# Kernel tuning notes

Hardware: AMD Instinct MI355X
Metric: run time of the kernel (lower is better)

## Reference

```python
import jax, jax.numpy as jnp
import numpy as np

N_NODES = 100000
N_EDGES = 20000  # hyperedges
NNZ = 800000
D = 128


def setup_inputs() -> dict:
    key = jax.random.key(0)
    ks = jax.random.split(key, 10)
    X = jax.random.normal(ks[0], (N_NODES, D), dtype=jnp.float32)
    X0 = jax.random.normal(ks[1], (N_NODES, D), dtype=jnp.float32)
    degE = jax.random.uniform(ks[2], (N_EDGES, 1), dtype=jnp.float32)
    degV = jax.random.uniform(ks[3], (N_NODES, 1), dtype=jnp.float32)
    alpha = jax.random.uniform(ks[4], (1,), dtype=jnp.float32)
    beta = jax.random.uniform(ks[5], (1,), dtype=jnp.float32)
    W_w = jax.random.normal(ks[6], (D, D), dtype=jnp.float32) / np.sqrt(D)
    g1_src = jax.random.randint(ks[7], (NNZ,), 0, N_NODES, dtype=jnp.int64 if jax.config.read('jax_enable_x64') else jnp.int32)
    g1_dst = jax.random.randint(ks[8], (NNZ,), 0, N_EDGES)
    g2_src = jax.random.randint(ks[9], (NNZ,), 0, N_EDGES)
    g2_dst = jax.random.randint(jax.random.fold_in(key, 99), (NNZ,), 0, N_NODES)
    return {"X": X, "X0": X0, "degE": degE, "degV": degV, "alpha": alpha,
            "beta": beta, "W_w": W_w, "g1_src": g1_src, "g1_dst": g1_dst,
            "g2_src": g2_src, "g2_dst": g2_dst}


def reference(X, X0, degE, degV, alpha, beta, W_w, g1_src, g1_dst, g2_src, g2_dst):
    n_edges = degE.shape[0]
    n_nodes = degV.shape[0]
    a = alpha[0]
    b = beta[0]
    # copy_u_sum(g1, X): gather node rows, scatter-sum into hyperedges
    Xe = jax.ops.segment_sum(X[g1_src], g1_dst, num_segments=n_edges)  # [E, D]
    Xe = Xe * degE
    # copy_u_sum(g2, Xe): gather hyperedge rows, scatter-sum into nodes
    Xv = jax.ops.segment_sum(Xe[g2_src], g2_dst, num_segments=n_nodes)  # [N, D]
    Xv = Xv * degV
    # GCNII-style initial residual + identity mapping
    Xi = (1.0 - a) * Xv + a * X0
    out = (1.0 - b) * Xi + b * (Xi @ W_w.T)  # Linear(bias=False)
    return out
```

## Files before the change

### kernel.cpp

```cpp
#include <hip/hip_runtime.h>

#define DD 128
#define SCAN_CHUNK 2048
#define PAD1 16
#define PAD2 8

typedef __attribute__((ext_vector_type(8))) _Float16 f16x8;
typedef __attribute__((ext_vector_type(4))) _Float16 f16x4;
typedef __attribute__((ext_vector_type(4))) float f32x4;

__global__ __launch_bounds__(256)
void k_hist1(const int* __restrict__ g1d, int* __restrict__ cnt1p,
             int* __restrict__ rank1, int nnz, int no, int hb,
             const float* __restrict__ W, const float* __restrict__ betaP,
             _Float16* __restrict__ Mh,
             const float* __restrict__ X, _Float16* __restrict__ Xh, int nx) {
    const int b = blockIdx.x;
    if (b < hb) {
        int q = b * 256 + threadIdx.x;
        if (q >= no) return;
        int i = q << 3;
        if (i + 8 <= nnz) {
            int4 d0 = *(const int4*)(g1d + i);
            int4 d1 = *(const int4*)(g1d + i + 4);
            int r0 = atomicAdd(&cnt1p[d0.x * PAD1], 1);
            int r1 = atomicAdd(&cnt1p[d0.y * PAD1], 1);
            int r2 = atomicAdd(&cnt1p[d0.z * PAD1], 1);
            int r3 = atomicAdd(&cnt1p[d0.w * PAD1], 1);
            int r4 = atomicAdd(&cnt1p[d1.x * PAD1], 1);
            int r5 = atomicAdd(&cnt1p[d1.y * PAD1], 1);
            int r6 = atomicAdd(&cnt1p[d1.z * PAD1], 1);
            int r7 = atomicAdd(&cnt1p[d1.w * PAD1], 1);
            *(int4*)(rank1 + i)     = make_int4(r0, r1, r2, r3);
            *(int4*)(rank1 + i + 4) = make_int4(r4, r5, r6, r7);
        } else {
            for (; i < nnz; ++i) rank1[i] = atomicAdd(&cnt1p[g1d[i] * PAD1], 1);
        }
        return;
    }
    if (b < hb + 8) {
        int gid = (b - hb) * 256 + threadIdx.x;
        if (gid >= DD * DD / 8) return;
        int c  = gid >> 4;
        int k0 = (gid & 15) << 3;
        float bb = betaP[0], ib = 1.0f - bb;
        const float* p = W + c * DD + k0;
        float4 lo = *(const float4*)p, hi = *(const float4*)(p + 4);
        float v[8] = {lo.x, lo.y, lo.z, lo.w, hi.x, hi.y, hi.z, hi.w};
        f16x8 t;
        #pragma unroll
        for (int j = 0; j < 8; ++j) {
            float m = bb * v[j] + ((k0 + j) == c ? ib : 0.0f);
            t[j] = (_Float16)m;
        }
        *(f16x8*)(Mh + (size_t)c * DD + k0) = t;
        return;
    }
    int gid = (b - hb - 8) * 256 + threadIdx.x;
    int i = gid << 3;
    if (i + 8 <= nx) {
        float4 lo = *(const float4*)(X + i);
        float4 hi = *(const float4*)(X + i + 4);
        f16x8 t;
        t[0] = (_Float16)lo.x; t[1] = (_Float16)lo.y;
        t[2] = (_Float16)lo.z; t[3] = (_Float16)lo.w;
        t[4] = (_Float16)hi.x; t[5] = (_Float16)hi.y;
        t[6] = (_Float16)hi.z; t[7] = (_Float16)hi.w;
        *(f16x8*)(Xh + i) = t;
    } else {
        for (; i < nx; ++i) Xh[i] = (_Float16)X[i];
    }
}

__global__ __launch_bounds__(256)
void k_scan_blocks(const int* __restrict__ cnt, int* __restrict__ off,
                   int* __restrict__ bsum, int n, int str) {
    __shared__ int sh[256];
    const int tid = threadIdx.x;
    const int base = blockIdx.x * SCAN_CHUNK + tid * 8;
    int v[8];
    int s = 0;
    #pragma unroll
    for (int j = 0; j < 8; ++j) {
        int idx = base + j;
        v[j] = (idx < n) ? cnt[(size_t)idx * str] : 0;
        s += v[j];
    }
    sh[tid] = s;
    __syncthreads();
    for (int d = 1; d < 256; d <<= 1) {
        int y = (tid >= d) ? sh[tid - d] : 0;
        __syncthreads();
        sh[tid] += y;
        __syncthreads();
    }
    int incl = sh[tid];
    int run = incl - s;
    #pragma unroll
    for (int j = 0; j < 8; ++j) {
        int idx = base + j;
        if (idx < n) off[idx] = run;
        run += v[j];
    }
    if (tid == 255) bsum[blockIdx.x] = incl;
}

__global__ __launch_bounds__(256)
void k_scan_add(int* __restrict__ off, const int* __restrict__ bsum,
                int n, int nnz) {
    int gid = blockIdx.x * 256 + threadIdx.x;
    if (gid == 0) off[n] = nnz;
    if (gid >= n) return;
    int chunk = gid >> 11;
    int p = 0;
    for (int i = 0; i < chunk; ++i) p += bsum[i];
    off[gid] += p;
}

__global__ __launch_bounds__(256)
void k_fill(const int* __restrict__ dst, const int* __restrict__ src,
            const int* __restrict__ off, const int* __restrict__ rank,
            int* __restrict__ out, int nnz) {
    int q = blockIdx.x * 256 + threadIdx.x;
    int i = q << 2;
    if (i + 4 <= nnz) {
        int4 d = *(const int4*)(dst + i);
        int4 s = *(const int4*)(src + i);
        int4 r = *(const int4*)(rank + i);
        int o0 = off[d.x];
        int o1 = off[d.y];
        int o2 = off[d.z];
        int o3 = off[d.w];
        out[o0 + r.x] = s.x;
        out[o1 + r.y] = s.y;
        out[o2 + r.z] = s.z;
        out[o3 + r.w] = s.w;
    } else {
        for (; i < nnz; ++i) out[off[dst[i]] + rank[i]] = src[i];
    }
}

__global__ __launch_bounds__(256)
void k_h2_egather(const int* __restrict__ g2d, int* __restrict__ cnt2p,
                  int* __restrict__ rank2, int nnz, int no, int H,
                  const _Float16* __restrict__ Xh, const int* __restrict__ off1,
                  const int* __restrict__ srcs1, const float* __restrict__ degE,
                  _Float16* __restrict__ XeH, int n_edges) {
    if (blockIdx.x < H) {
        int q = blockIdx.x * 256 + threadIdx.x;
        if (q >= no) return;
        int i = q << 3;
        if (i + 8 <= nnz) {
            int4 d0 = *(const int4*)(g2d + i);
            int4 d1 = *(const int4*)(g2d + i + 4);
            int r0 = atomicAdd(&cnt2p[d0.x * PAD2], 1);
            int r1 = atomicAdd(&cnt2p[d0.y * PAD2], 1);
            int r2 = atomicAdd(&cnt2p[d0.z * PAD2], 1);
            int r3 = atomicAdd(&cnt2p[d0.w * PAD2], 1);
            int r4 = atomicAdd(&cnt2p[d1.x * PAD2], 1);
            int r5 = atomicAdd(&cnt2p[d1.y * PAD2], 1);
            int r6 = atomicAdd(&cnt2p[d1.z * PAD2], 1);
            int r7 = atomicAdd(&cnt2p[d1.w * PAD2], 1);
            *(int4*)(rank2 + i)     = make_int4(r0, r1, r2, r3);
            *(int4*)(rank2 + i + 4) = make_int4(r4, r5, r6, r7);
        } else {
            for (; i < nnz; ++i) rank2[i] = atomicAdd(&cnt2p[g2d[i] * PAD2], 1);
        }
        return;
    }
    int gid = (blockIdx.x - H) * 256 + threadIdx.x;
    int e = gid >> 4;
    if (e >= n_edges) return;
    int k = (gid & 15) << 3;
    int beg = off1[e], end = off1[e + 1];
    float a0[8] = {0, 0, 0, 0, 0, 0, 0, 0};
    float a1[8] = {0, 0, 0, 0, 0, 0, 0, 0};
    int j = beg;
    for (; j + 8 <= end; j += 8) {
        int s0 = srcs1[j + 0];
        int s1 = srcs1[j + 1];
        int s2 = srcs1[j + 2];
        int s3 = srcs1[j + 3];
        int s4 = srcs1[j + 4];
        int s5 = srcs1[j + 5];
        int s6 = srcs1[j + 6];
        int s7 = srcs1[j + 7];
        f16x8 v0 = *(const f16x8*)(Xh + (size_t)s0 * DD + k);
        f16x8 v1 = *(const f16x8*)(Xh + (size_t)s1 * DD + k);
        f16x8 v2 = *(const f16x8*)(Xh + (size_t)s2 * DD + k);
        f16x8 v3 = *(const f16x8*)(Xh + (size_t)s3 * DD + k);
        f16x8 v4 = *(const f16x8*)(Xh + (size_t)s4 * DD + k);
        f16x8 v5 = *(const f16x8*)(Xh + (size_t)s5 * DD + k);
        f16x8 v6 = *(const f16x8*)(Xh + (size_t)s6 * DD + k);
        f16x8 v7 = *(const f16x8*)(Xh + (size_t)s7 * DD + k);
        #pragma unroll
        for (int t = 0; t < 8; ++t) {
            a0[t] += (float)v0[t] + (float)v2[t];
            a1[t] += (float)v1[t] + (float)v3[t];
        }
        #pragma unroll
        for (int t = 0; t < 8; ++t) {
            a0[t] += (float)v4[t] + (float)v6[t];
            a1[t] += (float)v5[t] + (float)v7[t];
        }
    }
    for (; j < end; ++j) {
        int s = srcs1[j];
        f16x8 v = *(const f16x8*)(Xh + (size_t)s * DD + k);
        #pragma unroll
        for (int t = 0; t < 8; ++t) a0[t] += (float)v[t];
    }
    float f = degE[e];
    f16x8 ob;
    #pragma unroll
    for (int t = 0; t < 8; ++t) ob[t] = (_Float16)(f * (a0[t] + a1[t]));
    *(f16x8*)(XeH + (size_t)e * DD + k) = ob;
}

__global__ __launch_bounds__(256)
void k_node_gather(const _Float16* __restrict__ XeH, const int* __restrict__ off,
                   const int* __restrict__ srcs, const float* __restrict__ degV,
                   const float* __restrict__ X0, const float* __restrict__ alphaP,
                   float* __restrict__ Xi, int n_nodes) {
    int gid = blockIdx.x * 256 + threadIdx.x;
    int v = gid >> 5;
    if (v >= n_nodes) return;
    int k = (gid & 31) << 2;
    int beg = off[v], end = off[v + 1];
    float4 acc0 = {0, 0, 0, 0}, acc1 = {0, 0, 0, 0};
    int j = beg;
    for (; j + 4 <= end; j += 4) {
        int s0 = srcs[j + 0];
        int s1 = srcs[j + 1];
        int s2 = srcs[j + 2];
        int s3 = srcs[j + 3];
        f16x4 h0 = *(const f16x4*)(XeH + (size_t)s0 * DD + k);
        f16x4 h1 = *(const f16x4*)(XeH + (size_t)s1 * DD + k);
        f16x4 h2 = *(const f16x4*)(XeH + (size_t)s2 * DD + k);
        f16x4 h3 = *(const f16x4*)(XeH + (size_t)s3 * DD + k);
        acc0.x += (float)h0[0]; acc0.y += (float)h0[1]; acc0.z += (float)h0[2]; acc0.w += (float)h0[3];
        acc1.x += (float)h1[0]; acc1.y += (float)h1[1]; acc1.z += (float)h1[2]; acc1.w += (float)h1[3];
        acc0.x += (float)h2[0]; acc0.y += (float)h2[1]; acc0.z += (float)h2[2]; acc0.w += (float)h2[3];
        acc1.x += (float)h3[0]; acc1.y += (float)h3[1]; acc1.z += (float)h3[2]; acc1.w += (float)h3[3];
    }
    for (; j < end; ++j) {
        int s = srcs[j];
        f16x4 h = *(const f16x4*)(XeH + (size_t)s * DD + k);
        acc0.x += (float)h[0]; acc0.y += (float)h[1]; acc0.z += (float)h[2]; acc0.w += (float)h[3];
    }
    float a = alphaP[0];
    float f = (1.0f - a) * degV[v];
    float4 x0 = *(const float4*)(X0 + (size_t)v * DD + k);
    float4 o;
    o.x = f * (acc0.x + acc1.x) + a * x0.x;
    o.y = f * (acc0.y + acc1.y) + a * x0.y;
    o.z = f * (acc0.z + acc1.z) + a * x0.z;
    o.w = f * (acc0.w + acc1.w) + a * x0.w;
    *(float4*)(Xi + (size_t)v * DD + k) = o;
}

__global__ __launch_bounds__(256)
void k_gemm_mfma(float* xio, const _Float16* __restrict__ Mh, int n_rows) {
    const int lane = threadIdx.x & 63;
    const int wid  = threadIdx.x >> 6;
    const int m16  = lane & 15;
    const int quad = lane >> 4;
    const int kq   = quad * 8;

    const int strip = blockIdx.x * 4 + wid;
    const int row0 = strip * 16;
    if (row0 >= n_rows) return;

    int arow = row0 + m16;
    if (arow >= n_rows) arow = n_rows - 1;
    const float* xr = xio + (size_t)arow * DD;

    f16x8 af[4];
    #pragma unroll
    for (int kf = 0; kf < 4; ++kf) {
        const float* p = xr + kf * 32 + kq;
        float4 lo = *(const float4*)p;
        float4 hi = *(const float4*)(p + 4);
        f16x8 t;
        t[0] = (_Float16)lo.x; t[1] = (_Float16)lo.y;
        t[2] = (_Float16)lo.z; t[3] = (_Float16)lo.w;
        t[4] = (_Float16)hi.x; t[5] = (_Float16)hi.y;
        t[6] = (_Float16)hi.z; t[7] = (_Float16)hi.w;
        af[kf] = t;
    }

    #pragma unroll
    for (int nt = 0; nt < 8; ++nt) {
        const _Float16* mr = Mh + (size_t)(nt * 16 + m16) * DD + kq;
        f32x4 acc = {0.f, 0.f, 0.f, 0.f};
        #pragma unroll
        for (int kf = 0; kf < 4; ++kf) {
            f16x8 bfrag = *(const f16x8*)(mr + kf * 32);
            acc = __builtin_amdgcn_mfma_f32_16x16x32_f16(af[kf], bfrag, acc, 0, 0, 0);
        }
        const int col = nt * 16 + m16;
        #pragma unroll
        for (int r = 0; r < 4; ++r) {
            int row = row0 + quad * 4 + r;
            if (row < n_rows)
                xio[(size_t)row * DD + col] = acc[r];
        }
    }
}

extern "C" void kernel_launch(void* const* d_in, const int* in_sizes, int n_in,
                              void* d_out, int out_size, void* d_ws, size_t ws_size,
                              hipStream_t stream) {
    const float* X     = (const float*)d_in[0];
    const float* X0    = (const float*)d_in[1];
    const float* degE  = (const float*)d_in[2];
    const float* degV  = (const float*)d_in[3];
    const float* alpha = (const float*)d_in[4];
    const float* beta  = (const float*)d_in[5];
    const float* W     = (const float*)d_in[6];
    const int*   g1s   = (const int*)d_in[7];
    const int*   g1d   = (const int*)d_in[8];
    const int*   g2s   = (const int*)d_in[9];
    const int*   g2d   = (const int*)d_in[10];
    float* out = (float*)d_out;

    const int n_nodes = in_sizes[3];
    const int n_edges = in_sizes[2];
    const int nnz     = in_sizes[7];
    const int nx      = n_nodes * DD;

    int*   wsi   = (int*)d_ws;
    _Float16* XeH = (_Float16*)d_ws;
    size_t o     = (size_t)n_edges * DD / 2;
    int*   rank1 = wsi + o;
    int*   rank2 = rank1;
    o += nnz;
    int*   off1  = wsi + o;          o += n_edges + 1;
    int*   off2  = wsi + o;          o += n_nodes + 1;
    size_t srcs_base = o;
    int*   srcs1 = wsi + o;          o += nnz;
    int*   srcs2 = wsi + o;          o += nnz;
    int*   bsum  = wsi + o;          o += 64;
    _Float16* Mh = (_Float16*)(wsi + o); o += DD * DD / 2;
    int*   cnt1p = wsi + srcs_base;
    int*   cnt2p = wsi + srcs_base + nnz;
    _Float16* Xh = (_Float16*)d_out;

    hipMemsetAsync(cnt1p, 0, 2 * (size_t)nnz * sizeof(int), stream);

    const int nb1 = (n_edges + SCAN_CHUNK - 1) / SCAN_CHUNK;
    const int nb2 = (n_nodes + SCAN_CHUNK - 1) / SCAN_CHUNK;
    const int no  = (nnz + 7) / 8;
    const int hb  = (no + 255) / 256;
    const int cb  = (nx / 8 + 255) / 256;
    const int nq  = (nnz + 3) / 4;
    const int qb  = (nq + 255) / 256;

    k_hist1<<<hb + 8 + cb, 256, 0, stream>>>(g1d, cnt1p, rank1, nnz, no, hb,
                                             W, beta, Mh, X, Xh, nx);
    k_scan_blocks<<<nb1, 256, 0, stream>>>(cnt1p, off1, bsum, n_edges, PAD1);
    k_scan_add<<<(n_edges + 255) / 256, 256, 0, stream>>>(off1, bsum, n_edges, nnz);
    k_fill<<<qb, 256, 0, stream>>>(g1d, g1s, off1, rank1, srcs1, nnz);

    const int egb = (n_edges * 16 + 255) / 256;
    k_h2_egather<<<hb + egb, 256, 0, stream>>>(g2d, cnt2p, rank2, nnz, no, hb,
                                               Xh, off1, srcs1, degE, XeH, n_edges);

    k_scan_blocks<<<nb2, 256, 0, stream>>>(cnt2p, off2, bsum, n_nodes, PAD2);
    k_scan_add<<<(n_nodes + 255) / 256, 256, 0, stream>>>(off2, bsum, n_nodes, nnz);
    k_fill<<<qb, 256, 0, stream>>>(g2d, g2s, off2, rank2, srcs2, nnz);

    k_node_gather<<<(n_nodes * 32 + 255) / 256, 256, 0, stream>>>(
        XeH, off2, srcs2, degV, X0, alpha, out, n_nodes);

    const int nstrips = (n_nodes + 15) / 16;
    k_gemm_mfma<<<(nstrips + 3) / 4, 256, 0, stream>>>(out, Mh, n_nodes);
}
```

Before: 374.8 us.

## Fuse node gather into MFMA GEMM, drop scan-add passes, wave-per-edge gather

Removes both k_scan_add kernels: each consumer block now builds the block-prefix array from bsum in shared memory and adds it to the local scan offsets. The node gather is fused into the MFMA GEMM. Each wave accumulates a 16-row strip, writes Xi as fp16 into swizzled LDS and feeds the MFMA directly, so the fp32 Xi round trip through global memory goes away. The edge gather changes from 16 lanes per edge to a full wave per edge, with four sub-groups reduced by shuffles. Costs are a serial per-block prefix loop, less parallelism per node in the gather (4 lanes per row), and extra register pressure from 32 accumulators.

```diff
diff --git a/kernel.cpp b/kernel.cpp
--- a/kernel.cpp
+++ b/kernel.cpp
@@ -99,44 +99,41 @@
     #pragma unroll
     for (int j = 0; j < 8; ++j) {
         int idx = base + j;
-        if (idx < n) off[idx] = run;
+        if (idx <= n) off[idx] = run;
         run += v[j];
     }
     if (tid == 255) bsum[blockIdx.x] = incl;
-}
-
-__global__ __launch_bounds__(256)
-void k_scan_add(int* __restrict__ off, const int* __restrict__ bsum,
-                int n, int nnz) {
-    int gid = blockIdx.x * 256 + threadIdx.x;
-    if (gid == 0) off[n] = nnz;
-    if (gid >= n) return;
-    int chunk = gid >> 11;
-    int p = 0;
-    for (int i = 0; i < chunk; ++i) p += bsum[i];
-    off[gid] += p;
 }
 
 __global__ __launch_bounds__(256)
 void k_fill(const int* __restrict__ dst, const int* __restrict__ src,
             const int* __restrict__ off, const int* __restrict__ rank,
+            const int* __restrict__ bsum, int nb,
             int* __restrict__ out, int nnz) {
+    __shared__ int pref[64];
+    if (threadIdx.x == 0) {
+        int run = 0;
+        for (int i = 0; i < nb; ++i) { pref[i] = run; run += bsum[i]; }
+        pref[nb] = run;
+    }
+    __syncthreads();
     int q = blockIdx.x * 256 + threadIdx.x;
     int i = q << 2;
     if (i + 4 <= nnz) {
         int4 d = *(const int4*)(dst + i);
         int4 s = *(const int4*)(src + i);
         int4 r = *(const int4*)(rank + i);
-        int o0 = off[d.x];
-        int o1 = off[d.y];
-        int o2 = off[d.z];
-        int o3 = off[d.w];
+        int o0 = off[d.x] + pref[d.x >> 11];
+        int o1 = off[d.y] + pref[d.y >> 11];
+        int o2 = off[d.z] + pref[d.z >> 11];
+        int o3 = off[d.w] + pref[d.w >> 11];
         out[o0 + r.x] = s.x;
         out[o1 + r.y] = s.y;
         out[o2 + r.z] = s.z;
         out[o3 + r.w] = s.w;
     } else {
-        for (; i < nnz; ++i) out[off[dst[i]] + rank[i]] = src[i];
+        for (; i < nnz; ++i)
+            out[off[dst[i]] + pref[dst[i] >> 11] + rank[i]] = src[i];
     }
 }
 
@@ -144,6 +141,7 @@
 void k_h2_egather(const int* __restrict__ g2d, int* __restrict__ cnt2p,
                   int* __restrict__ rank2, int nnz, int no, int H,
                   const _Float16* __restrict__ Xh, const int* __restrict__ off1,
+                  const int* __restrict__ bsum1, int nb1,
                   const int* __restrict__ srcs1, const float* __restrict__ degE,
                   _Float16* __restrict__ XeH, int n_edges) {
     if (blockIdx.x < H) {
@@ -168,127 +166,167 @@
         }
         return;
     }
-    int gid = (blockIdx.x - H) * 256 + threadIdx.x;
-    int e = gid >> 4;
+    __shared__ int pref[16];
+    if (threadIdx.x == 0) {
+        int run = 0;
+        for (int i = 0; i < nb1; ++i) { pref[i] = run; run += bsum1[i]; }
+        pref[nb1] = run;
+    }
+    __syncthreads();
+    const int wid  = threadIdx.x >> 6;
+    const int lane = threadIdx.x & 63;
+    int e = (blockIdx.x - H) * 4 + wid;
     if (e >= n_edges) return;
-    int k = (gid & 15) << 3;
-    int beg = off1[e], end = off1[e + 1];
+    const int g = lane >> 4;
+    const int c = lane & 15;
+    int beg = off1[e] + pref[e >> 11];
+    int end = off1[e + 1] + pref[(e + 1) >> 11];
     float a0[8] = {0, 0, 0, 0, 0, 0, 0, 0};
     float a1[8] = {0, 0, 0, 0, 0, 0, 0, 0};
-    int j = beg;
-    for (; j + 8 <= end; j += 8) {
-        int s0 = srcs1[j + 0];
-        int s1 = srcs1[j + 1];
-        int s2 = srcs1[j + 2];
-        int s3 = srcs1[j + 3];
-        int s4 = srcs1[j + 4];
-        int s5 = srcs1[j + 5];
-        int s6 = srcs1[j + 6];
-        int s7 = srcs1[j + 7];
-        f16x8 v0 = *(const f16x8*)(Xh + (size_t)s0 * DD + k);
-        f16x8 v1 = *(const f16x8*)(Xh + (size_t)s1 * DD + k);
-        f16x8 v2 = *(const f16x8*)(Xh + (size_t)s2 * DD + k);
-        f16x8 v3 = *(const f16x8*)(Xh + (size_t)s3 * DD + k);
-        f16x8 v4 = *(const f16x8*)(Xh + (size_t)s4 * DD + k);
-        f16x8 v5 = *(const f16x8*)(Xh + (size_t)s5 * DD + k);
-        f16x8 v6 = *(const f16x8*)(Xh + (size_t)s6 * DD + k);
-        f16x8 v7 = *(const f16x8*)(Xh + (size_t)s7 * DD + k);
-        #pragma unroll
-        for (int t = 0; t < 8; ++t) {
-            a0[t] += (float)v0[t] + (float)v2[t];
-            a1[t] += (float)v1[t] + (float)v3[t];
-        }
-        #pragma unroll
-        for (int t = 0; t < 8; ++t) {
-            a0[t] += (float)v4[t] + (float)v6[t];
-            a1[t] += (float)v5[t] + (float)v7[t];
-        }
-    }
-    for (; j < end; ++j) {
+    int j = beg + g;
+    for (; j + 4 < end; j += 8) {
+        int s0 = srcs1[j];
+        int s1 = srcs1[j + 4];
+        f16x8 v0 = *(const f16x8*)(Xh + (size_t)s0 * DD + c * 8);
+        f16x8 v1 = *(const f16x8*)(Xh + (size_t)s1 * DD + c * 8);
+        #pragma unroll
+        for (int t = 0; t < 8; ++t) { a0[t] += (float)v0[t]; a1[t] += (float)v1[t]; }
+    }
+    if (j < end) {
         int s = srcs1[j];
-        f16x8 v = *(const f16x8*)(Xh + (size_t)s * DD + k);
+        f16x8 v = *(const f16x8*)(Xh + (size_t)s * DD + c * 8);
         #pragma unroll
         for (int t = 0; t < 8; ++t) a0[t] += (float)v[t];
     }
-    float f = degE[e];
-    f16x8 ob;
-    #pragma unroll
-    for (int t = 0; t < 8; ++t) ob[t] = (_Float16)(f * (a0[t] + a1[t]));
-    *(f16x8*)(XeH + (size_t)e * DD + k) = ob;
+    float r[8];
+    #pragma unroll
+    for (int t = 0; t < 8; ++t) r[t] = a0[t] + a1[t];
+    #pragma unroll
+    for (int t = 0; t < 8; ++t) r[t] += __shfl_xor(r[t], 16);
+    #pragma unroll
+    for (int t = 0; t < 8; ++t) r[t] += __shfl_xor(r[t], 32);
+    if (g == 0) {
+        float f = degE[e];
+        f16x8 ob;
+        #pragma unroll
+        for (int t = 0; t < 8; ++t) ob[t] = (_Float16)(f * r[t]);
+        *(f16x8*)(XeH + (size_t)e * DD + c * 8) = ob;
+    }
 }
 
 __global__ __launch_bounds__(256)
-void k_node_gather(const _Float16* __restrict__ XeH, const int* __restrict__ off,
-                   const int* __restrict__ srcs, const float* __restrict__ degV,
-                   const float* __restrict__ X0, const float* __restrict__ alphaP,
-                   float* __restrict__ Xi, int n_nodes) {
-    int gid = blockIdx.x * 256 + threadIdx.x;
-    int v = gid >> 5;
-    if (v >= n_nodes) return;
-    int k = (gid & 31) << 2;
-    int beg = off[v], end = off[v + 1];
-    float4 acc0 = {0, 0, 0, 0}, acc1 = {0, 0, 0, 0};
-    int j = beg;
-    for (; j + 4 <= end; j += 4) {
-        int s0 = srcs[j + 0];
-        int s1 = srcs[j + 1];
-        int s2 = srcs[j + 2];
-        int s3 = srcs[j + 3];
-        f16x4 h0 = *(const f16x4*)(XeH + (size_t)s0 * DD + k);
-        f16x4 h1 = *(const f16x4*)(XeH + (size_t)s1 * DD + k);
-        f16x4 h2 = *(const f16x4*)(XeH + (size_t)s2 * DD + k);
-        f16x4 h3 = *(const f16x4*)(XeH + (size_t)s3 * DD + k);
-        acc0.x += (float)h0[0]; acc0.y += (float)h0[1]; acc0.z += (float)h0[2]; acc0.w += (float)h0[3];
-        acc1.x += (float)h1[0]; acc1.y += (float)h1[1]; acc1.z += (float)h1[2]; acc1.w += (float)h1[3];
-        acc0.x += (float)h2[0]; acc0.y += (float)h2[1]; acc0.z += (float)h2[2]; acc0.w += (float)h2[3];
-        acc1.x += (float)h3[0]; acc1.y += (float)h3[1]; acc1.z += (float)h3[2]; acc1.w += (float)h3[3];
-    }
-    for (; j < end; ++j) {
-        int s = srcs[j];
-        f16x4 h = *(const f16x4*)(XeH + (size_t)s * DD + k);
-        acc0.x += (float)h[0]; acc0.y += (float)h[1]; acc0.z += (float)h[2]; acc0.w += (float)h[3];
-    }
-    float a = alphaP[0];
-    float f = (1.0f - a) * degV[v];
-    float4 x0 = *(const float4*)(X0 + (size_t)v * DD + k);
-    float4 o;
-    o.x = f * (acc0.x + acc1.x) + a * x0.x;
-    o.y = f * (acc0.y + acc1.y) + a * x0.y;
-    o.z = f * (acc0.z + acc1.z) + a * x0.z;
-    o.w = f * (acc0.w + acc1.w) + a * x0.w;
-    *(float4*)(Xi + (size_t)v * DD + k) = o;
-}
-
-__global__ __launch_bounds__(256)
-void k_gemm_mfma(float* xio, const _Float16* __restrict__ Mh, int n_rows) {
-    const int lane = threadIdx.x & 63;
-    const int wid  = threadIdx.x >> 6;
+void k_ng_gemm(const _Float16* __restrict__ XeH, const int* __restrict__ off2,
+               const int* __restrict__ bsum2, int nb2,
+               const int* __restrict__ srcs2, const float* __restrict__ degV,
+               const float* __restrict__ X0, const float* __restrict__ alphaP,
+               const _Float16* __restrict__ Mh, float* __restrict__ out,
+               int n_nodes) {
+    __shared__ int pref[64];
+    __shared__ _Float16 xi_lds[4][16 * DD];
+    const int tid = threadIdx.x;
+    if (tid == 0) {
+        int run = 0;
+        for (int i = 0; i < nb2; ++i) { pref[i] = run; run += bsum2[i]; }
+        pref[nb2] = run;
+    }
+    __syncthreads();
+    const int wid  = tid >> 6;
+    const int lane = tid & 63;
+    const int strip = blockIdx.x * 4 + wid;
+    const int row0 = strip * 16;
+    const bool live = row0 < n_nodes;
+    _Float16* lbase = &xi_lds[wid][0];
+
+    const int r16 = lane >> 2;
+    const int sl  = lane & 3;
+    const int row = row0 + r16;
+    if (live) {
+        float acc[32];
+        #pragma unroll
+        for (int t = 0; t < 32; ++t) acc[t] = 0.0f;
+        if (row < n_nodes) {
+            int beg = off2[row] + pref[row >> 11];
+            int end = off2[row + 1] + pref[(row + 1) >> 11];
+            int j = beg;
+            for (; j + 2 <= end; j += 2) {
+                int s0 = srcs2[j];
+                int s1 = srcs2[j + 1];
+                const _Float16* p0 = XeH + (size_t)s0 * DD + sl * 32;
+                const _Float16* p1 = XeH + (size_t)s1 * DD + sl * 32;
+                f16x8 u0 = *(const f16x8*)(p0);
+                f16x8 u1 = *(const f16x8*)(p0 + 8);
+                f16x8 u2 = *(const f16x8*)(p0 + 16);
+                f16x8 u3 = *(const f16x8*)(p0 + 24);
+                f16x8 w0 = *(const f16x8*)(p1);
+                f16x8 w1 = *(const f16x8*)(p1 + 8);
+                f16x8 w2 = *(const f16x8*)(p1 + 16);
+                f16x8 w3 = *(const f16x8*)(p1 + 24);
+                #pragma unroll
+                for (int t = 0; t < 8; ++t) {
+                    acc[t]      += (float)u0[t] + (float)w0[t];
+                    acc[8 + t]  += (float)u1[t] + (float)w1[t];
+                    acc[16 + t] += (float)u2[t] + (float)w2[t];
+                    acc[24 + t] += (float)u3[t] + (float)w3[t];
+                }
+            }
+            if (j < end) {
+                int s = srcs2[j];
+                const _Float16* p0 = XeH + (size_t)s * DD + sl * 32;
+                f16x8 u0 = *(const f16x8*)(p0);
+                f16x8 u1 = *(const f16x8*)(p0 + 8);
+                f16x8 u2 = *(const f16x8*)(p0 + 16);
+                f16x8 u3 = *(const f16x8*)(p0 + 24);
+                #pragma unroll
+                for (int t = 0; t < 8; ++t) {
+                    acc[t]      += (float)u0[t];
+                    acc[8 + t]  += (float)u1[t];
+                    acc[16 + t] += (float)u2[t];
+                    acc[24 + t] += (float)u3[t];
+                }
+            }
+            float a = alphaP[0];
+            float f = (1.0f - a) * degV[row];
+            const float* x0p = X0 + (size_t)row * DD + sl * 32;
+            #pragma unroll
+            for (int c2 = 0; c2 < 4; ++c2) {
+                float4 xa = *(const float4*)(x0p + c2 * 8);
+                float4 xb = *(const float4*)(x0p + c2 * 8 + 4);
+                f16x8 h;
+                h[0] = (_Float16)(f * acc[c2 * 8 + 0] + a * xa.x);
+                h[1] = (_Float16)(f * acc[c2 * 8 + 1] + a * xa.y);
+                h[2] = (_Float16)(f * acc[c2 * 8 + 2] + a * xa.z);
+                h[3] = (_Float16)(f * acc[c2 * 8 + 3] + a * xa.w);
+                h[4] = (_Float16)(f * acc[c2 * 8 + 4] + a * xb.x);
+                h[5] = (_Float16)(f * acc[c2 * 8 + 5] + a * xb.y);
+                h[6] = (_Float16)(f * acc[c2 * 8 + 6] + a * xb.z);
+                h[7] = (_Float16)(f * acc[c2 * 8 + 7] + a * xb.w);
+                int byte = r16 * 256 + sl * 64 + c2 * 16;
+                byte ^= (r16 & 7) << 4;
+                *(f16x8*)((char*)lbase + byte) = h;
+            }
+        } else {
+            f16x8 z = {0, 0, 0, 0, 0, 0, 0, 0};
+            #pragma unroll
+            for (int c2 = 0; c2 < 4; ++c2) {
+                int byte = r16 * 256 + sl * 64 + c2 * 16;
+                byte ^= (r16 & 7) << 4;
+                *(f16x8*)((char*)lbase + byte) = z;
+            }
+        }
+    }
+    __syncthreads();
+    if (!live) return;
+
     const int m16  = lane & 15;
     const int quad = lane >> 4;
     const int kq   = quad * 8;
-
-    const int strip = blockIdx.x * 4 + wid;
-    const int row0 = strip * 16;
-    if (row0 >= n_rows) return;
-
-    int arow = row0 + m16;
-    if (arow >= n_rows) arow = n_rows - 1;
-    const float* xr = xio + (size_t)arow * DD;
-
     f16x8 af[4];
     #pragma unroll
     for (int kf = 0; kf < 4; ++kf) {
-        const float* p = xr + kf * 32 + kq;
-        float4 lo = *(const float4*)p;
-        float4 hi = *(const float4*)(p + 4);
-        f16x8 t;
-        t[0] = (_Float16)lo.x; t[1] = (_Float16)lo.y;
-        t[2] = (_Float16)lo.z; t[3] = (_Float16)lo.w;
-        t[4] = (_Float16)hi.x; t[5] = (_Float16)hi.y;
-        t[6] = (_Float16)hi.z; t[7] = (_Float16)hi.w;
-        af[kf] = t;
-    }
-
+        int byte = m16 * 256 + kf * 64 + quad * 16;
+        byte ^= (m16 & 7) << 4;
+        af[kf] = *(const f16x8*)((const char*)lbase + byte);
+    }
     #pragma unroll
     for (int nt = 0; nt < 8; ++nt) {
         const _Float16* mr = Mh + (size_t)(nt * 16 + m16) * DD + kq;
@@ -301,9 +339,9 @@
         const int col = nt * 16 + m16;
         #pragma unroll
         for (int r = 0; r < 4; ++r) {
-            int row = row0 + quad * 4 + r;
-            if (row < n_rows)
-                xio[(size_t)row * DD + col] = acc[r];
+            int orow = row0 + quad * 4 + r;
+            if (orow < n_nodes)
+                out[(size_t)orow * DD + col] = acc[r];
         }
     }
 }
@@ -340,7 +378,7 @@
     size_t srcs_base = o;
     int*   srcs1 = wsi + o;          o += nnz;
     int*   srcs2 = wsi + o;          o += nnz;
-    int*   bsum  = wsi + o;          o += 64;
+    int*   bsum  = wsi + o;          o += 128;
     _Float16* Mh = (_Float16*)(wsi + o); o += DD * DD / 2;
     int*   cnt1p = wsi + srcs_base;
     int*   cnt2p = wsi + srcs_base + nnz;
@@ -359,20 +397,17 @@
     k_hist1<<<hb + 8 + cb, 256, 0, stream>>>(g1d, cnt1p, rank1, nnz, no, hb,
                                              W, beta, Mh, X, Xh, nx);
     k_scan_blocks<<<nb1, 256, 0, stream>>>(cnt1p, off1, bsum, n_edges, PAD1);
-    k_scan_add<<<(n_edges + 255) / 256, 256, 0, stream>>>(off1, bsum, n_edges, nnz);
-    k_fill<<<qb, 256, 0, stream>>>(g1d, g1s, off1, rank1, srcs1, nnz);
-
-    const int egb = (n_edges * 16 + 255) / 256;
+    k_fill<<<qb, 256, 0, stream>>>(g1d, g1s, off1, rank1, bsum, nb1, srcs1, nnz);
+
+    const int egb = (n_edges + 3) / 4;
     k_h2_egather<<<hb + egb, 256, 0, stream>>>(g2d, cnt2p, rank2, nnz, no, hb,
-                                               Xh, off1, srcs1, degE, XeH, n_edges);
-
-    k_scan_blocks<<<nb2, 256, 0, stream>>>(cnt2p, off2, bsum, n_nodes, PAD2);
-    k_scan_add<<<(n_nodes + 255) / 256, 256, 0, stream>>>(off2, bsum, n_nodes, nnz);
-    k_fill<<<qb, 256, 0, stream>>>(g2d, g2s, off2, rank2, srcs2, nnz);
-
-    k_node_gather<<<(n_nodes * 32 + 255) / 256, 256, 0, stream>>>(
-        XeH, off2, srcs2, degV, X0, alpha, out, n_nodes);
+                                               Xh, off1, bsum, nb1,
+                                               srcs1, degE, XeH, n_edges);
+
+    k_scan_blocks<<<nb2, 256, 0, stream>>>(cnt2p, off2, bsum + 64, n_nodes, PAD2);
+    k_fill<<<qb, 256, 0, stream>>>(g2d, g2s, off2, rank2, bsum + 64, nb2, srcs2, nnz);
 
     const int nstrips = (n_nodes + 15) / 16;
-    k_gemm_mfma<<<(nstrips + 3) / 4, 256, 0, stream>>>(out, Mh, n_nodes);
-}
+    k_ng_gemm<<<(nstrips + 3) / 4, 256, 0, stream>>>(
+        XeH, off2, bsum + 64, nb2, srcs2, degV, X0, alpha, Mh, out, n_nodes);
+}
```

After: 354.6 us. 1.06x faster.
